# Kernel optimization log

Measured on AMD Instinct MI355X. Metric: run time of the kernel, lower is better.

Reference implementation:

```python
import jax, jax.numpy as jnp
import numpy as np

N_NODES = 50000
N_EDGES = 1600000
IN_FEAT = 128
HIDDEN = 128
CLASSES = 2


def gin_conv(x, src, dst, W, b, n_nodes):
    # GINConv (eps=0): h_i = mlp(x_i + sum_{j in N(i)} x_j)
    agg = jax.ops.segment_sum(x[src], dst, num_segments=n_nodes)  # [N, F]
    h = x + agg
    return h @ W + b


def setup_inputs() -> dict:
    key = jax.random.key(0)
    ks = jax.random.split(key, 8)
    x = jax.random.normal(ks[0], (N_NODES, IN_FEAT), dtype=jnp.float32)
    edge_index = jax.random.randint(ks[1], (2, N_EDGES), 0, N_NODES, dtype=jnp.int64)
    def lin(k, fan_in, fan_out):
        kw, kb = jax.random.split(k)
        bound = 1.0 / np.sqrt(fan_in)
        W = jax.random.uniform(kw, (fan_in, fan_out), jnp.float32, -bound, bound)
        b = jax.random.uniform(kb, (fan_out,), jnp.float32, -bound, bound)
        return W, b
    W1, b1 = lin(ks[2], IN_FEAT, HIDDEN)
    W2, b2 = lin(ks[3], HIDDEN, HIDDEN)
    W3, b3 = lin(ks[4], HIDDEN, CLASSES)
    return {"x": x, "edge_index": edge_index, "W1": W1, "b1": b1,
            "W2": W2, "b2": b2, "W3": W3, "b3": b3}


def reference(x, edge_index, W1, b1, W2, b2, W3, b3):
    src, dst = edge_index[0], edge_index[1]
    n = x.shape[0]
    h = jax.nn.relu(gin_conv(x, src, dst, W1, b1, n))
    h = jax.nn.relu(gin_conv(h, src, dst, W2, b2, n))
    return gin_conv(h, src, dst, W3, b3, n)
```

## Files before the change

### kernel.cpp

```cpp
#include <hip/hip_runtime.h>

#define NNODES 50000
#define NEDGES 1600000
#define F 128

#define NB 128
#define BSH 391
#define BCAP 13312
#define EPT 10

typedef __attribute__((ext_vector_type(8))) short bf16x8;
typedef __attribute__((ext_vector_type(4))) float f32x4;

__device__ inline unsigned short f2bf(float f) {
    union { float f; unsigned u; } v; v.f = f;
    unsigned r = v.u + 0x7FFF + ((v.u >> 16) & 1);
    return (unsigned short)(r >> 16);
}
__device__ inline float2 up2(ushort2 h) {
    union { unsigned u; float f; } a, b;
    a.u = ((unsigned)h.x) << 16; b.u = ((unsigned)h.y) << 16;
    return make_float2(a.f, b.f);
}

__global__ __launch_bounds__(256) void cvt_bf16(const float4* __restrict__ in,
                                                ushort4* __restrict__ out, int n4) {
    int i = blockIdx.x * blockDim.x + threadIdx.x;
    int stride = gridDim.x * blockDim.x;
    for (; i < n4; i += stride) {
        float4 v = in[i];
        ushort4 o;
        o.x = f2bf(v.x); o.y = f2bf(v.y); o.z = f2bf(v.z); o.w = f2bf(v.w);
        out[i] = o;
    }
}

__global__ __launch_bounds__(256) void wprep2(const float* __restrict__ W1,
                                              const float* __restrict__ W2,
                                              unsigned short* __restrict__ Wf1,
                                              unsigned short* __restrict__ Wf2,
                                              int* __restrict__ gcnt) {
    int id = blockIdx.x * 256 + threadIdx.x;
    if (blockIdx.x == 0 && threadIdx.x < NB) gcnt[threadIdx.x] = 0;
    const float* W = (id < 2048) ? W1 : W2;
    unsigned short* Wf = (id < 2048) ? Wf1 : Wf2;
    id &= 2047;
    const int l = id & 63, nn = (id >> 6) & 7, s = id >> 9;
    const int c = nn * 16 + (l & 15);
    const int k0 = s * 32 + (l >> 4) * 8;
    ushort4 lo, hi;
    lo.x = f2bf(W[(k0 + 0) * F + c]); lo.y = f2bf(W[(k0 + 1) * F + c]);
    lo.z = f2bf(W[(k0 + 2) * F + c]); lo.w = f2bf(W[(k0 + 3) * F + c]);
    hi.x = f2bf(W[(k0 + 4) * F + c]); hi.y = f2bf(W[(k0 + 5) * F + c]);
    hi.z = f2bf(W[(k0 + 6) * F + c]); hi.w = f2bf(W[(k0 + 7) * F + c]);
    ushort4* p = (ushort4*)(Wf + (size_t)id * 8);
    p[0] = lo; p[1] = hi;
}

__global__ __launch_bounds__(256) void bucketA(const int* __restrict__ src,
                                               const int* __restrict__ dst,
                                               unsigned* __restrict__ E1,
                                               int* __restrict__ gcnt) {
    __shared__ unsigned hist[4][NB];
    __shared__ unsigned start[4][NB];
    const int t = threadIdx.x, w = t >> 6;
    for (int i = t; i < 4 * NB; i += 256) ((unsigned*)hist)[i] = 0;
    __syncthreads();
    const int base = blockIdx.x * (256 * EPT);
    unsigned rec[EPT]; int bkt[EPT];
#pragma unroll
    for (int k = 0; k < EPT; ++k) {
        const int i = base + k * 256 + t;
        const int s = src[i], d = dst[i];
        const int b = d / BSH;
        rec[k] = ((unsigned)s << 9) | (unsigned)(d - b * BSH);
        bkt[k] = b;
        atomicAdd(&hist[w][b], 1u);
    }
    __syncthreads();
    if (t < NB) {
        const unsigned h0 = hist[0][t], h1 = hist[1][t], h2 = hist[2][t], h3 = hist[3][t];
        const unsigned tot = h0 + h1 + h2 + h3;
        const unsigned g = tot ? (unsigned)atomicAdd(&gcnt[t], (int)tot) : 0u;
        start[0][t] = g;
        start[1][t] = g + h0;
        start[2][t] = g + h0 + h1;
        start[3][t] = g + h0 + h1 + h2;
        hist[0][t] = 0; hist[1][t] = 0; hist[2][t] = 0; hist[3][t] = 0;
    }
    __syncthreads();
#pragma unroll
    for (int k = 0; k < EPT; ++k) {
        const int b = bkt[k];
        const unsigned p = start[w][b] + atomicAdd(&hist[w][b], 1u);
        if (p < BCAP) E1[(size_t)b * BCAP + p] = rec[k];
    }
}

__global__ __launch_bounds__(256) void bucketB(const unsigned* __restrict__ E1,
                                               const int* __restrict__ gcnt,
                                               int* __restrict__ off,
                                               unsigned short* __restrict__ ssrc) {
    __shared__ int cnt[BSH];
    __shared__ int cur[BSH];
    __shared__ int wtot[4];
    __shared__ int bst[NB];
    const int b = blockIdx.x, t = threadIdx.x;
    if (t < 64) {
        const int a0 = gcnt[t * 2], a1 = gcnt[t * 2 + 1];
        const int s = a0 + a1;
        int inc = s;
#pragma unroll
        for (int o = 1; o <= 32; o <<= 1) {
            int u = __shfl_up(inc, o);
            if (t >= o) inc += u;
        }
        bst[t * 2] = inc - s;
        bst[t * 2 + 1] = inc - s + a0;
    }
    for (int i = t; i < BSH; i += 256) cnt[i] = 0;
    __syncthreads();
    const int ne = min(gcnt[b], BCAP);
    const int ebase = bst[b];
    const unsigned* E = E1 + (size_t)b * BCAP;
    for (int i = t; i < ne; i += 256) atomicAdd(&cnt[E[i] & 511], 1);
    __syncthreads();
    const int i0 = t * 2, i1 = t * 2 + 1;
    const int a0 = (i0 < BSH) ? cnt[i0] : 0;
    const int a1 = (i1 < BSH) ? cnt[i1] : 0;
    const int s = a0 + a1;
    int inc = s;
    const int lane = t & 63, w = t >> 6;
#pragma unroll
    for (int o = 1; o <= 32; o <<= 1) {
        int u = __shfl_up(inc, o);
        if (lane >= o) inc += u;
    }
    if (lane == 63) wtot[w] = inc;
    __syncthreads();
    int woff = 0;
    for (int k = 0; k < w; ++k) woff += wtot[k];
    const int excl = woff + inc - s;
    if (i0 < BSH) {
        cur[i0] = excl;
        const int n = b * BSH + i0;
        if (n < NNODES) off[n] = ebase + excl;
    }
    if (i1 < BSH) {
        cur[i1] = excl + a0;
        const int n = b * BSH + i1;
        if (n < NNODES) off[n] = ebase + excl + a0;
    }
    if (b == NB - 1 && t == 0) off[NNODES] = NEDGES;
    __syncthreads();
    for (int i = t; i < ne; i += 256) {
        const unsigned rec = E[i];
        const int r = atomicAdd(&cur[rec & 511], 1);
        ssrc[ebase + r] = (unsigned short)(rec >> 9);
    }
}

__global__ __launch_bounds__(256) void agg_bf16(const ushort2* __restrict__ h,
                                                const int* __restrict__ off,
                                                const unsigned short* __restrict__ ssrc,
                                                ushort2* __restrict__ S, int n) {
    const int wid = (blockIdx.x * blockDim.x + threadIdx.x) >> 6;
    const int lane = threadIdx.x & 63;
    if (wid >= n) return;
    const int e0 = off[wid], e1 = off[wid + 1];
    float2 acc = up2(h[(size_t)wid * 64 + lane]);
    for (int base = e0; base < e1; base += 64) {
        const int cnt = min(64, e1 - base);
        const int myidx = (base + lane < e1) ? (int)ssrc[base + lane] : 0;
        int i = 0;
        for (; i + 8 <= cnt; i += 8) {
            const int s0 = __shfl(myidx, i + 0), s1 = __shfl(myidx, i + 1);
            const int s2 = __shfl(myidx, i + 2), s3 = __shfl(myidx, i + 3);
            const int s4 = __shfl(myidx, i + 4), s5 = __shfl(myidx, i + 5);
            const int s6 = __shfl(myidx, i + 6), s7 = __shfl(myidx, i + 7);
            const float2 v0 = up2(h[(size_t)s0 * 64 + lane]);
            const float2 v1 = up2(h[(size_t)s1 * 64 + lane]);
            const float2 v2 = up2(h[(size_t)s2 * 64 + lane]);
            const float2 v3 = up2(h[(size_t)s3 * 64 + lane]);
            const float2 v4 = up2(h[(size_t)s4 * 64 + lane]);
            const float2 v5 = up2(h[(size_t)s5 * 64 + lane]);
            const float2 v6 = up2(h[(size_t)s6 * 64 + lane]);
            const float2 v7 = up2(h[(size_t)s7 * 64 + lane]);
            acc.x += ((v0.x + v1.x) + (v2.x + v3.x)) + ((v4.x + v5.x) + (v6.x + v7.x));
            acc.y += ((v0.y + v1.y) + (v2.y + v3.y)) + ((v4.y + v5.y) + (v6.y + v7.y));
        }
        for (; i < cnt; ++i) {
            const int s = __shfl(myidx, i);
            const float2 v = up2(h[(size_t)s * 64 + lane]);
            acc.x += v.x;
            acc.y += v.y;
        }
    }
    ushort2 o;
    o.x = f2bf(acc.x); o.y = f2bf(acc.y);
    S[(size_t)wid * 64 + lane] = o;
}

__global__ __launch_bounds__(256) void mlp_mfma(const unsigned short* __restrict__ Sb,
                                                const unsigned short* __restrict__ Wfrag,
                                                const float* __restrict__ bias,
                                                unsigned short* __restrict__ Hb,
                                                int n, int relu) {
    const int wave = threadIdx.x >> 6, lane = threadIdx.x & 63;
    const int base = blockIdx.x * 64 + wave * 16;
    const int r16 = lane & 15, hi = lane >> 4;
    int arow = base + r16;
    if (arow >= n) arow = n - 1;
    const unsigned short* Arow = Sb + (size_t)arow * F;

    f32x4 acc[8];
#pragma unroll
    for (int i = 0; i < 8; ++i) acc[i] = (f32x4){0.f, 0.f, 0.f, 0.f};

#pragma unroll
    for (int s = 0; s < 4; ++s) {
        const bf16x8 a = *(const bf16x8*)(Arow + s * 32 + hi * 8);
#pragma unroll
        for (int nn = 0; nn < 8; ++nn) {
            const bf16x8 b = *(const bf16x8*)(Wfrag + ((size_t)(s * 8 + nn) * 64 + lane) * 8);
            acc[nn] = __builtin_amdgcn_mfma_f32_16x16x32_bf16(a, b, acc[nn], 0, 0, 0);
        }
    }

#pragma unroll
    for (int nn = 0; nn < 8; ++nn) {
        const int col = nn * 16 + r16;
        const float bv = bias[col];
#pragma unroll
        for (int r = 0; r < 4; ++r) {
            const int row = base + hi * 4 + r;
            if (row < n) {
                float v = acc[nn][r] + bv;
                if (relu) v = fmaxf(v, 0.f);
                Hb[(size_t)row * F + col] = f2bf(v);
            }
        }
    }
}

__global__ __launch_bounds__(256) void head_t(const ushort2* __restrict__ Hb,
                                              const float4* __restrict__ W3,
                                              float2* __restrict__ y, int n) {
    const int wid = (blockIdx.x * blockDim.x + threadIdx.x) >> 6;
    const int lane = threadIdx.x & 63;
    if (wid >= n) return;
    const float2 h = up2(Hb[(size_t)wid * 64 + lane]);
    const float4 w = W3[lane];
    float a0 = h.x * w.x + h.y * w.z;
    float a1 = h.x * w.y + h.y * w.w;
#pragma unroll
    for (int o = 32; o; o >>= 1) {
        a0 += __shfl_xor(a0, o);
        a1 += __shfl_xor(a1, o);
    }
    if (lane == 0) y[wid] = make_float2(a0, a1);
}

__global__ __launch_bounds__(256) void agg3(const float2* __restrict__ y,
                                            const int* __restrict__ off,
                                            const unsigned short* __restrict__ ssrc,
                                            const float* __restrict__ b3,
                                            float2* __restrict__ out, int n) {
    const int i = blockIdx.x * blockDim.x + threadIdx.x;
    if (i >= n) return;
    float2 acc = y[i];
    const int e1 = off[i + 1];
    for (int e = off[i]; e < e1; ++e) {
        const float2 v = y[ssrc[e]];
        acc.x += v.x;
        acc.y += v.y;
    }
    out[i] = make_float2(acc.x + b3[0], acc.y + b3[1]);
}

extern "C" void kernel_launch(void* const* d_in, const int* in_sizes, int n_in,
                              void* d_out, int out_size, void* d_ws, size_t ws_size,
                              hipStream_t stream) {
    const float* x  = (const float*)d_in[0];
    const int* ei   = (const int*)d_in[1];
    const int* src  = ei;
    const int* dst  = ei + NEDGES;
    const float* W1 = (const float*)d_in[2];
    const float* b1 = (const float*)d_in[3];
    const float* W2 = (const float*)d_in[4];
    const float* b2 = (const float*)d_in[5];
    const float* W3 = (const float*)d_in[6];
    const float* b3 = (const float*)d_in[7];
    float* out = (float*)d_out;

    char* ws = (char*)d_ws;
    const size_t featB = (size_t)NNODES * F * 2;
    unsigned short* xb = (unsigned short*)ws;
    unsigned short* Sb = (unsigned short*)(ws + featB);
    unsigned short* Hb = (unsigned short*)(ws + 2 * featB);
    char* p = ws + 3 * featB;
    float* y3 = (float*)p;                 p += (size_t)NNODES * 2 * 4 + 256;
    unsigned short* Wf1 = (unsigned short*)p; p += 2048 * 8 * 2;
    unsigned short* Wf2 = (unsigned short*)p; p += 2048 * 8 * 2;
    unsigned* E1 = (unsigned*)p;           p += (size_t)NB * BCAP * 4;
    int* gcnt = (int*)p;                   p += NB * 4 + 256;
    int* off = (int*)p;                    p += (size_t)(NNODES + 1) * 4 + 256;
    unsigned short* ssrc = (unsigned short*)p;

    cvt_bf16<<<1024, 256, 0, stream>>>((const float4*)x, (ushort4*)xb, NNODES * F / 4);
    wprep2<<<16, 256, 0, stream>>>(W1, W2, Wf1, Wf2, gcnt);

    bucketA<<<NEDGES / (256 * EPT), 256, 0, stream>>>(src, dst, E1, gcnt);
    bucketB<<<NB, 256, 0, stream>>>(E1, gcnt, off, ssrc);

    const int aggBlocks = (NNODES + 3) / 4;
    const int mlpBlocks = (NNODES + 63) / 64;

    agg_bf16<<<aggBlocks, 256, 0, stream>>>((const ushort2*)xb, off, ssrc, (ushort2*)Sb, NNODES);
    mlp_mfma<<<mlpBlocks, 256, 0, stream>>>(Sb, Wf1, b1, Hb, NNODES, 1);

    agg_bf16<<<aggBlocks, 256, 0, stream>>>((const ushort2*)Hb, off, ssrc, (ushort2*)Sb, NNODES);
    mlp_mfma<<<mlpBlocks, 256, 0, stream>>>(Sb, Wf2, b2, xb, NNODES, 1);

    head_t<<<aggBlocks, 256, 0, stream>>>((const ushort2*)xb, (const float4*)W3, (float2*)y3, NNODES);
    agg3<<<(NNODES + 255) / 256, 256, 0, stream>>>((const float2*)y3, off, ssrc, b3, (float2*)out, NNODES);
}
```

Measured before the change: 291.3 us.

## Double bucket count, reuse atomic ranks, widen gather unroll, one-wave agg blocks

Bucketing now uses 256 buckets of 196 nodes, so each bucketB block does less work and the grid is larger. bucketA keeps the rank returned by the first histogram atomic instead of zeroing and redoing the atomics in the scatter pass. The aggregation kernel runs as one 64-thread block per node and gathers 16 neighbours per batch to keep more loads in flight. head_t switches to scalar bf16 loads, a cosmetic change. The costs are higher register pressure from the 16-wide gather and more, smaller blocks to schedule.

```diff
diff --git a/kernel.cpp b/kernel.cpp
--- a/kernel.cpp
+++ b/kernel.cpp
@@ -4,9 +4,9 @@
 #define NEDGES 1600000
 #define F 128
 
-#define NB 128
-#define BSH 391
-#define BCAP 13312
+#define NB 256
+#define BSH 196
+#define BCAP 6784
 #define EPT 10
 
 typedef __attribute__((ext_vector_type(8))) short bf16x8;
@@ -21,6 +21,11 @@
     union { unsigned u; float f; } a, b;
     a.u = ((unsigned)h.x) << 16; b.u = ((unsigned)h.y) << 16;
     return make_float2(a.f, b.f);
+}
+__device__ inline float b2f(unsigned short h) {
+    union { unsigned u; float f; } a;
+    a.u = ((unsigned)h) << 16;
+    return a.f;
 }
 
 __global__ __launch_bounds__(256) void cvt_bf16(const float4* __restrict__ in,
@@ -41,7 +46,7 @@
                                               unsigned short* __restrict__ Wf2,
                                               int* __restrict__ gcnt) {
     int id = blockIdx.x * 256 + threadIdx.x;
-    if (blockIdx.x == 0 && threadIdx.x < NB) gcnt[threadIdx.x] = 0;
+    if (blockIdx.x == 0) gcnt[threadIdx.x] = 0;
     const float* W = (id < 2048) ? W1 : W2;
     unsigned short* Wf = (id < 2048) ? Wf1 : Wf2;
     id &= 2047;
@@ -67,18 +72,18 @@
     for (int i = t; i < 4 * NB; i += 256) ((unsigned*)hist)[i] = 0;
     __syncthreads();
     const int base = blockIdx.x * (256 * EPT);
-    unsigned rec[EPT]; int bkt[EPT];
+    unsigned rec[EPT]; int bkt[EPT]; unsigned rnk[EPT];
 #pragma unroll
     for (int k = 0; k < EPT; ++k) {
         const int i = base + k * 256 + t;
         const int s = src[i], d = dst[i];
         const int b = d / BSH;
-        rec[k] = ((unsigned)s << 9) | (unsigned)(d - b * BSH);
+        rec[k] = ((unsigned)s << 8) | (unsigned)(d - b * BSH);
         bkt[k] = b;
-        atomicAdd(&hist[w][b], 1u);
-    }
-    __syncthreads();
-    if (t < NB) {
+        rnk[k] = atomicAdd(&hist[w][b], 1u);
+    }
+    __syncthreads();
+    {
         const unsigned h0 = hist[0][t], h1 = hist[1][t], h2 = hist[2][t], h3 = hist[3][t];
         const unsigned tot = h0 + h1 + h2 + h3;
         const unsigned g = tot ? (unsigned)atomicAdd(&gcnt[t], (int)tot) : 0u;
@@ -86,14 +91,12 @@
         start[1][t] = g + h0;
         start[2][t] = g + h0 + h1;
         start[3][t] = g + h0 + h1 + h2;
-        hist[0][t] = 0; hist[1][t] = 0; hist[2][t] = 0; hist[3][t] = 0;
     }
     __syncthreads();
 #pragma unroll
     for (int k = 0; k < EPT; ++k) {
-        const int b = bkt[k];
-        const unsigned p = start[w][b] + atomicAdd(&hist[w][b], 1u);
-        if (p < BCAP) E1[(size_t)b * BCAP + p] = rec[k];
+        const unsigned p = start[w][bkt[k]] + rnk[k];
+        if (p < BCAP) E1[(size_t)bkt[k] * BCAP + p] = rec[k];
     }
 }
 
@@ -107,29 +110,30 @@
     __shared__ int bst[NB];
     const int b = blockIdx.x, t = threadIdx.x;
     if (t < 64) {
-        const int a0 = gcnt[t * 2], a1 = gcnt[t * 2 + 1];
-        const int s = a0 + a1;
+        const int a0 = gcnt[t * 4], a1 = gcnt[t * 4 + 1];
+        const int a2 = gcnt[t * 4 + 2], a3 = gcnt[t * 4 + 3];
+        const int s = a0 + a1 + a2 + a3;
         int inc = s;
 #pragma unroll
         for (int o = 1; o <= 32; o <<= 1) {
             int u = __shfl_up(inc, o);
             if (t >= o) inc += u;
         }
-        bst[t * 2] = inc - s;
-        bst[t * 2 + 1] = inc - s + a0;
+        const int e = inc - s;
+        bst[t * 4] = e;
+        bst[t * 4 + 1] = e + a0;
+        bst[t * 4 + 2] = e + a0 + a1;
+        bst[t * 4 + 3] = e + a0 + a1 + a2;
     }
     for (int i = t; i < BSH; i += 256) cnt[i] = 0;
     __syncthreads();
     const int ne = min(gcnt[b], BCAP);
     const int ebase = bst[b];
     const unsigned* E = E1 + (size_t)b * BCAP;
-    for (int i = t; i < ne; i += 256) atomicAdd(&cnt[E[i] & 511], 1);
-    __syncthreads();
-    const int i0 = t * 2, i1 = t * 2 + 1;
-    const int a0 = (i0 < BSH) ? cnt[i0] : 0;
-    const int a1 = (i1 < BSH) ? cnt[i1] : 0;
-    const int s = a0 + a1;
-    int inc = s;
+    for (int i = t; i < ne; i += 256) atomicAdd(&cnt[E[i] & 255], 1);
+    __syncthreads();
+    const int val = (t < BSH) ? cnt[t] : 0;
+    int inc = val;
     const int lane = t & 63, w = t >> 6;
 #pragma unroll
     for (int o = 1; o <= 32; o <<= 1) {
@@ -140,54 +144,54 @@
     __syncthreads();
     int woff = 0;
     for (int k = 0; k < w; ++k) woff += wtot[k];
-    const int excl = woff + inc - s;
-    if (i0 < BSH) {
-        cur[i0] = excl;
-        const int n = b * BSH + i0;
+    const int excl = woff + inc - val;
+    if (t < BSH) {
+        cur[t] = excl;
+        const int n = b * BSH + t;
         if (n < NNODES) off[n] = ebase + excl;
-    }
-    if (i1 < BSH) {
-        cur[i1] = excl + a0;
-        const int n = b * BSH + i1;
-        if (n < NNODES) off[n] = ebase + excl + a0;
     }
     if (b == NB - 1 && t == 0) off[NNODES] = NEDGES;
     __syncthreads();
     for (int i = t; i < ne; i += 256) {
         const unsigned rec = E[i];
-        const int r = atomicAdd(&cur[rec & 511], 1);
-        ssrc[ebase + r] = (unsigned short)(rec >> 9);
-    }
-}
-
-__global__ __launch_bounds__(256) void agg_bf16(const ushort2* __restrict__ h,
-                                                const int* __restrict__ off,
-                                                const unsigned short* __restrict__ ssrc,
-                                                ushort2* __restrict__ S, int n) {
-    const int wid = (blockIdx.x * blockDim.x + threadIdx.x) >> 6;
-    const int lane = threadIdx.x & 63;
-    if (wid >= n) return;
+        const int r = atomicAdd(&cur[rec & 255], 1);
+        ssrc[ebase + r] = (unsigned short)(rec >> 8);
+    }
+}
+
+__global__ __launch_bounds__(64) void agg_bf16(const ushort2* __restrict__ h,
+                                               const int* __restrict__ off,
+                                               const unsigned short* __restrict__ ssrc,
+                                               ushort2* __restrict__ S, int n) {
+    const int wid = blockIdx.x;
+    const int lane = threadIdx.x;
     const int e0 = off[wid], e1 = off[wid + 1];
     float2 acc = up2(h[(size_t)wid * 64 + lane]);
     for (int base = e0; base < e1; base += 64) {
         const int cnt = min(64, e1 - base);
         const int myidx = (base + lane < e1) ? (int)ssrc[base + lane] : 0;
         int i = 0;
-        for (; i + 8 <= cnt; i += 8) {
+        for (; i + 16 <= cnt; i += 16) {
+            float2 v[16];
+#pragma unroll
+            for (int k = 0; k < 16; ++k) {
+                const int s = __shfl(myidx, i + k);
+                v[k] = up2(h[(size_t)s * 64 + lane]);
+            }
+            float x0 = 0.f, y0 = 0.f;
+#pragma unroll
+            for (int k = 0; k < 16; ++k) { x0 += v[k].x; y0 += v[k].y; }
+            acc.x += x0; acc.y += y0;
+        }
+        for (; i + 4 <= cnt; i += 4) {
             const int s0 = __shfl(myidx, i + 0), s1 = __shfl(myidx, i + 1);
             const int s2 = __shfl(myidx, i + 2), s3 = __shfl(myidx, i + 3);
-            const int s4 = __shfl(myidx, i + 4), s5 = __shfl(myidx, i + 5);
-            const int s6 = __shfl(myidx, i + 6), s7 = __shfl(myidx, i + 7);
             const float2 v0 = up2(h[(size_t)s0 * 64 + lane]);
             const float2 v1 = up2(h[(size_t)s1 * 64 + lane]);
             const float2 v2 = up2(h[(size_t)s2 * 64 + lane]);
             const float2 v3 = up2(h[(size_t)s3 * 64 + lane]);
-            const float2 v4 = up2(h[(size_t)s4 * 64 + lane]);
-            const float2 v5 = up2(h[(size_t)s5 * 64 + lane]);
-            const float2 v6 = up2(h[(size_t)s6 * 64 + lane]);
-            const float2 v7 = up2(h[(size_t)s7 * 64 + lane]);
-            acc.x += ((v0.x + v1.x) + (v2.x + v3.x)) + ((v4.x + v5.x) + (v6.x + v7.x));
-            acc.y += ((v0.y + v1.y) + (v2.y + v3.y)) + ((v4.y + v5.y) + (v6.y + v7.y));
+            acc.x += (v0.x + v1.x) + (v2.x + v3.x);
+            acc.y += (v0.y + v1.y) + (v2.y + v3.y);
         }
         for (; i < cnt; ++i) {
             const int s = __shfl(myidx, i);
@@ -243,16 +247,17 @@
     }
 }
 
-__global__ __launch_bounds__(256) void head_t(const ushort2* __restrict__ Hb,
+__global__ __launch_bounds__(256) void head_t(const unsigned short* __restrict__ Hb,
                                               const float4* __restrict__ W3,
                                               float2* __restrict__ y, int n) {
     const int wid = (blockIdx.x * blockDim.x + threadIdx.x) >> 6;
     const int lane = threadIdx.x & 63;
     if (wid >= n) return;
-    const float2 h = up2(Hb[(size_t)wid * 64 + lane]);
+    const unsigned short* hp = Hb + (size_t)wid * F + lane * 2;
+    const float hx = b2f(hp[0]), hy = b2f(hp[1]);
     const float4 w = W3[lane];
-    float a0 = h.x * w.x + h.y * w.z;
-    float a1 = h.x * w.y + h.y * w.w;
+    float a0 = hx * w.x + hy * w.z;
+    float a1 = hx * w.y + hy * w.w;
 #pragma unroll
     for (int o = 32; o; o >>= 1) {
         a0 += __shfl_xor(a0, o);
@@ -313,15 +318,14 @@
     bucketA<<<NEDGES / (256 * EPT), 256, 0, stream>>>(src, dst, E1, gcnt);
     bucketB<<<NB, 256, 0, stream>>>(E1, gcnt, off, ssrc);
 
-    const int aggBlocks = (NNODES + 3) / 4;
     const int mlpBlocks = (NNODES + 63) / 64;
 
-    agg_bf16<<<aggBlocks, 256, 0, stream>>>((const ushort2*)xb, off, ssrc, (ushort2*)Sb, NNODES);
+    agg_bf16<<<NNODES, 64, 0, stream>>>((const ushort2*)xb, off, ssrc, (ushort2*)Sb, NNODES);
     mlp_mfma<<<mlpBlocks, 256, 0, stream>>>(Sb, Wf1, b1, Hb, NNODES, 1);
 
-    agg_bf16<<<aggBlocks, 256, 0, stream>>>((const ushort2*)Hb, off, ssrc, (ushort2*)Sb, NNODES);
+    agg_bf16<<<NNODES, 64, 0, stream>>>((const ushort2*)Hb, off, ssrc, (ushort2*)Sb, NNODES);
     mlp_mfma<<<mlpBlocks, 256, 0, stream>>>(Sb, Wf2, b2, xb, NNODES, 1);
 
-    head_t<<<aggBlocks, 256, 0, stream>>>((const ushort2*)xb, (const float4*)W3, (float2*)y3, NNODES);
+    head_t<<<(NNODES + 3) / 4, 256, 0, stream>>>(xb, (const float4*)W3, (float2*)y3, NNODES);
     agg3<<<(NNODES + 255) / 256, 256, 0, stream>>>((const float2*)y3, off, ssrc, b3, (float2*)out, NNODES);
 }
```

Result: faster. 276.3 us (-5.2%).
